# Performance work log

Hardware: AMD Instinct MI355X
Metric: run time of the kernel (lower is better)

## Reference

```python
import jax, jax.numpy as jnp
import numpy as np

NP = 100000   # total patch-graph nodes
NG = 2000     # number of patch graphs == mesh nodes
EP = 800000   # patch edges
NM = 2000     # mesh nodes
EM = 32000    # mesh edges
FIN = 5       # patch_feat_dim
EPS = 1e-5


def _leaky(x, s):
    return jnp.where(x >= 0, x, s * x)


def _gat(x, W, al, ar, src, dst, n):
    # DGL GATConv (no bias/residual, eval mode): per-head projection,
    # additive attention with LeakyReLU(0.2), segment softmax over incoming
    # edges per destination, weighted scatter-sum.
    H, D = al.shape
    h = (x @ W).reshape(n, H, D)                  # [N,H,D]
    el = (h * al).sum(-1)                         # [N,H]
    er = (h * ar).sum(-1)                         # [N,H]
    e = _leaky(el[src] + er[dst], 0.2)            # [E,H]
    m = jax.ops.segment_max(e, dst, num_segments=n)
    ee = jnp.exp(e - m[dst])
    s = jax.ops.segment_sum(ee, dst, num_segments=n)
    a = ee / jnp.maximum(s, 1e-9)[dst]            # [E,H]
    return jax.ops.segment_sum(h[src] * a[:, :, None], dst, num_segments=n)


def _gnorm(x, g, b, al):
    # GraphNorm over all nodes in the batch (called without graph in source)
    mu = x.mean(0, keepdims=True)
    xc = x - al * mu
    v = (xc * xc).mean(0, keepdims=True)
    return g * xc / jnp.sqrt(v + EPS) + b


def setup_inputs() -> dict:
    key = jax.random.key(0)
    ks = jax.random.split(key, 40)
    w = lambda k, sh: jax.random.normal(k, sh, jnp.float32) * 0.1
    d = {}
    d['node_feats'] = jax.random.normal(ks[0], (NP, FIN), jnp.float32)
    d['patch_src'] = jax.random.randint(ks[1], (EP,), 0, NP)
    d['patch_dst'] = jax.random.randint(ks[2], (EP,), 0, NP)
    d['patch_gid'] = jnp.repeat(jnp.arange(NG), NP // NG)  # 50 nodes/graph
    d['mesh_src'] = jax.random.randint(ks[3], (EM,), 0, NM)
    d['mesh_dst'] = jax.random.randint(ks[4], (EM,), 0, NM)
    # PatchReader2GATLayer (hidden=64): GAT1 4h x64, GAT2 3h x64, GATcls 2h x32
    d['pW1'] = w(ks[5], (FIN, 256)); d['pal1'] = w(ks[6], (4, 64)); d['par1'] = w(ks[7], (4, 64))
    d['pg1_g'] = jnp.ones((256,)); d['pg1_b'] = jnp.zeros((256,)); d['pg1_a'] = jnp.ones((256,))
    d['pW2'] = w(ks[8], (256, 192)); d['pal2'] = w(ks[9], (3, 64)); d['par2'] = w(ks[10], (3, 64))
    d['pg2_g'] = jnp.ones((192,)); d['pg2_b'] = jnp.zeros((192,)); d['pg2_a'] = jnp.ones((192,))
    d['pW3'] = w(ks[11], (192, 64)); d['pal3'] = w(ks[12], (2, 32)); d['par3'] = w(ks[13], (2, 32))
    d['pcls'] = w(ks[14], (32, 32))
    # GraphNormPatchReader (readout_dim=32)
    d['rn_g'] = jnp.ones((32,)); d['rn_b'] = jnp.zeros((32,)); d['rn_a'] = jnp.ones((32,))
    # GraphMeshReader2GATLayer (hidden=64): GAT1 4h x64, GAT2 3h x32, GATcls 2h x32
    d['mW1'] = w(ks[15], (32, 256)); d['mal1'] = w(ks[16], (4, 64)); d['mar1'] = w(ks[17], (4, 64))
    d['mg1_g'] = jnp.ones((256,)); d['mg1_b'] = jnp.zeros((256,)); d['mg1_a'] = jnp.ones((256,))
    d['mW2'] = w(ks[18], (256, 96)); d['mal2'] = w(ks[19], (3, 32)); d['mar2'] = w(ks[20], (3, 32))
    d['mg2_g'] = jnp.ones((96,)); d['mg2_b'] = jnp.zeros((96,)); d['mg2_a'] = jnp.ones((96,))
    d['mW3'] = w(ks[21], (96, 64)); d['mal3'] = w(ks[22], (2, 32)); d['mar3'] = w(ks[23], (2, 32))
    d['mcls'] = w(ks[24], (32, 15))
    return d


def reference(node_feats, patch_src, patch_dst, patch_gid, mesh_src, mesh_dst,
              pW1, pal1, par1, pg1_g, pg1_b, pg1_a,
              pW2, pal2, par2, pg2_g, pg2_b, pg2_a,
              pW3, pal3, par3, pcls, rn_g, rn_b, rn_a,
              mW1, mal1, mar1, mg1_g, mg1_b, mg1_a,
              mW2, mal2, mar2, mg2_g, mg2_b, mg2_a,
              mW3, mal3, mar3, mcls):
    # ---- PatchReader2GATLayer over all batched patch graphs ----
    h = _gat(node_feats, pW1, pal1, par1, patch_src, patch_dst, NP).reshape(NP, -1)
    h = _gnorm(_leaky(h, 0.01), pg1_g, pg1_b, pg1_a)
    h = _gat(h, pW2, pal2, par2, patch_src, patch_dst, NP).reshape(NP, -1)
    h = _gnorm(_leaky(h, 0.01), pg2_g, pg2_b, pg2_a)
    h = _gat(h, pW3, pal3, par3, patch_src, patch_dst, NP).mean(1)  # [NP,32]
    cnt = jax.ops.segment_sum(jnp.ones((NP,), h.dtype), patch_gid, num_segments=NG)
    ro = jax.ops.segment_sum(h, patch_gid, num_segments=NG) / jnp.maximum(cnt, 1.0)[:, None]
    ro = ro @ pcls                                 # [NG,32] per-patch readouts
    ro = _gnorm(_leaky(ro, 0.01), rn_g, rn_b, rn_a)
    # ---- GraphMeshReader2GATLayer over mesh graph ----
    m = _gat(ro, mW1, mal1, mar1, mesh_src, mesh_dst, NM).reshape(NM, -1)
    m = _gnorm(_leaky(m, 0.01), mg1_g, mg1_b, mg1_a)
    m = _gat(m, mW2, mal2, mar2, mesh_src, mesh_dst, NM).reshape(NM, -1)
    m = _gnorm(_leaky(m, 0.01), mg2_g, mg2_b, mg2_a)
    m = _gat(m, mW3, mal3, mar3, mesh_src, mesh_dst, NM).mean(1)    # [NM,32]
    mesh_out = m.mean(0, keepdims=True) @ mcls     # dgl.mean_nodes -> [1,15]
    return (mesh_out, ro)
```

## Files before the change

kernel.cpp:

```cpp
#include <hip/hip_runtime.h>

typedef unsigned short ushort;
typedef unsigned int uint;
typedef __attribute__((ext_vector_type(8))) short short8;
typedef __attribute__((ext_vector_type(4))) float float4v;

#define DEV __device__ __forceinline__

DEV float b2f(ushort u) {
    union { uint i; float f; } v; v.i = ((uint)u) << 16; return v.f;
}
DEV ushort f2b(float f) {
    union { float f; uint i; } v; v.f = f;
    uint x = v.i;
    uint r = x + 0x7fffu + ((x >> 16) & 1u);
    return (ushort)(r >> 16);
}
DEV float leaky(float x, float s) { return x >= 0.f ? x : s * x; }

DEV void gload16(const void* g, void* l) {
    __builtin_amdgcn_global_load_lds((const __attribute__((address_space(1))) void*)g,
                                     (__attribute__((address_space(3))) void*)l, 16, 0, 0);
}

struct ConvArgs {
    const void* s[37];
    float* d[37];
    int n[37];
};

__global__ __launch_bounds__(256) void convert_kernel(ConvArgs a, const ushort* __restrict__ x0,
                                                      int* __restrict__ flag) {
    __shared__ int sfp32;
    int tid = threadIdx.x;
    if (tid < 64) {
        int cnt = 0;
        for (int j = 0; j < 8; j++) {
            ushort u = x0[(tid * 8 + j) * 2];
            int e = (u >> 7) & 0xFF;
            if (e >= 100 && e <= 140) cnt++;
        }
#pragma unroll
        for (int m = 1; m < 64; m <<= 1) cnt += __shfl_xor(cnt, m, 64);
        if (tid == 0) sfp32 = (cnt < 256) ? 1 : 0;
    }
    __syncthreads();
    bool fp32 = (sfp32 != 0);
    if (blockIdx.x == 0 && blockIdx.y == 0 && tid == 0) *flag = fp32 ? 1 : 0;

    int ai = blockIdx.y;
    int n = a.n[ai];
    const void* s = a.s[ai];
    float* d = a.d[ai];
    int stride = gridDim.x * blockDim.x;
    if (s == nullptr) {
        for (int i = blockIdx.x * blockDim.x + tid; i < n; i += stride) d[i] = 0.f;
    } else {
        for (int i = blockIdx.x * blockDim.x + tid; i < n; i += stride)
            d[i] = fp32 ? ((const float*)s)[i] : b2f(((const ushort*)s)[i]);
    }
}

struct PackArgs { const float* W; ushort* O; int K; int N; };
struct Pack5 { PackArgs m[5]; };

__global__ __launch_bounds__(256) void pack5_kernel(Pack5 pa) {
    int mi = blockIdx.y;
    const float* __restrict__ W = pa.m[mi].W;
    ushort* __restrict__ O = pa.m[mi].O;
    int K = pa.m[mi].K, N = pa.m[mi].N;
    int G = (K >> 3) * N;
    for (int gi = blockIdx.x * 256 + threadIdx.x; gi < G; gi += gridDim.x * 256) {
        int kb = gi / N;
        int n = gi - kb * N;
        const float* wp = W + (size_t)(kb * 8) * N + n;
        uint4 pk;
        pk.x = (uint)f2b(wp[0]) | ((uint)f2b(wp[N]) << 16);
        pk.y = (uint)f2b(wp[2 * N]) | ((uint)f2b(wp[3 * N]) << 16);
        pk.z = (uint)f2b(wp[4 * N]) | ((uint)f2b(wp[5 * N]) << 16);
        pk.w = (uint)f2b(wp[6 * N]) | ((uint)f2b(wp[7 * N]) << 16);
        *(uint4*)(O + (size_t)gi * 8) = pk;
    }
}

__global__ __launch_bounds__(64) void prep_elr_kernel(const float* __restrict__ W,
                                                      const float* __restrict__ al,
                                                      const float* __restrict__ ar,
                                                      float* __restrict__ wal,
                                                      float* __restrict__ war) {
    int t = threadIdx.x;
    if (t < 20) {
        int k = t >> 2, h = t & 3;
        float sl = 0.f, sr = 0.f;
        for (int d = 0; d < 64; d++) {
            float w = W[k * 256 + h * 64 + d];
            sl += w * al[h * 64 + d];
            sr += w * ar[h * 64 + d];
        }
        wal[t] = sl;
        war[t] = sr;
    }
}

__global__ __launch_bounds__(256) void hist_both(const int* __restrict__ dstP, int* __restrict__ cntP, int EPc,
                                                 const int* __restrict__ dstM, int* __restrict__ cntM, int EMc,
                                                 int PB) {
    bool patch = (int)blockIdx.x < PB;
    const int* dst = patch ? dstP : dstM;
    int* cnt = patch ? cntP : cntM;
    int E = patch ? EPc : EMc;
    int nb = patch ? PB : gridDim.x - PB;
    int b = patch ? blockIdx.x : blockIdx.x - PB;
    int stride = nb * blockDim.x;
    for (int i = b * blockDim.x + threadIdx.x; i < E; i += stride)
        atomicAdd(&cnt[dst[i]], 1);
}

__global__ __launch_bounds__(256) void scan_both(const int* __restrict__ cntP, int* __restrict__ offP,
                                                 int* __restrict__ bsumP, int nP, int SBP,
                                                 const int* __restrict__ cntM, int* __restrict__ offM,
                                                 int* __restrict__ bsumM, int nM) {
    __shared__ int ls[256];
    bool patch = (int)blockIdx.x < SBP;
    const int* cnt = patch ? cntP : cntM;
    int* off = patch ? offP : offM;
    int* bsum = patch ? bsumP : bsumM;
    int n = patch ? nP : nM;
    int b = patch ? blockIdx.x : blockIdx.x - SBP;
    int t = threadIdx.x;
    int base = b * 2048 + t * 8;
    int v[8];
    int s = 0;
#pragma unroll
    for (int i = 0; i < 8; i++) {
        int idx = base + i;
        v[i] = idx < n ? cnt[idx] : 0;
        s += v[i];
    }
    ls[t] = s;
    __syncthreads();
#pragma unroll
    for (int d = 1; d < 256; d <<= 1) {
        int add = (t >= d) ? ls[t - d] : 0;
        __syncthreads();
        ls[t] += add;
        __syncthreads();
    }
    int run = ls[t] - s;
#pragma unroll
    for (int i = 0; i < 8; i++) {
        int idx = base + i;
        if (idx < n) off[idx] = run;
        run += v[i];
// ... 33 lines not shown
                                                    int* __restrict__ csrM, int EMc, int PB) {
    bool patch = (int)blockIdx.x < PB;
    const int* src = patch ? srcP : srcM;
    const int* dst = patch ? dstP : dstM;
    const int* off = patch ? offP : offM;
    int* cursor = patch ? curP : curM;
    int* csr = patch ? csrP : csrM;
    int E = patch ? EPc : EMc;
    int nb = patch ? PB : gridDim.x - PB;
    int b = patch ? blockIdx.x : blockIdx.x - PB;
    int stride = nb * blockDim.x;
    for (int i = b * blockDim.x + threadIdx.x; i < E; i += stride) {
        int d = dst[i];
        int pos = off[d] + atomicAdd(&cursor[d], 1);
        csr[pos] = src[i];
    }
}

__global__ __launch_bounds__(256) void proj1b_kernel(const float* __restrict__ x,
                                                     const float* __restrict__ wal,
                                                     const float* __restrict__ war,
                                                     float* __restrict__ el,
                                                     float* __restrict__ er, int Nn) {
    int n = blockIdx.x * 256 + threadIdx.x;
    if (n >= Nn) return;
    float xv[5];
#pragma unroll
    for (int k = 0; k < 5; k++) xv[k] = x[n * 5 + k];
    float l0 = 0.f, l1 = 0.f, l2 = 0.f, l3 = 0.f;
    float r0 = 0.f, r1 = 0.f, r2 = 0.f, r3 = 0.f;
#pragma unroll
    for (int k = 0; k < 5; k++) {
        float xk = xv[k];
        l0 += xk * wal[k * 4 + 0];
        l1 += xk * wal[k * 4 + 1];
        l2 += xk * wal[k * 4 + 2];
        l3 += xk * wal[k * 4 + 3];
        r0 += xk * war[k * 4 + 0];
        r1 += xk * war[k * 4 + 1];
        r2 += xk * war[k * 4 + 2];
        r3 += xk * war[k * 4 + 3];
    }
    *(float4*)(el + n * 4) = make_float4(l0, l1, l2, l3);
    *(float4*)(er + n * 4) = make_float4(r0, r1, r2, r3);
}

__global__ __launch_bounds__(256, 4) void aggr1_fly_kernel(const float* __restrict__ x,
                                                           const float* __restrict__ W,
                                                           const float* __restrict__ el,
                                                           const float* __restrict__ er,
                                                           const int* __restrict__ off,
                                                           const int* __restrict__ csr,
                                                           float* __restrict__ out,
                                                           float* __restrict__ cstat, int Nn) {
    __shared__ float s1m[4][256];
    __shared__ float s1q[4][256];
    int wid = threadIdx.x >> 6;
    int lane = threadIdx.x & 63;
    int grp = lane / 20;
    int gl = lane - grp * 20;
    int dbase = blockIdx.x * 12 + wid * 3;
    int d = dbase + grp;
    bool accl = (grp < 3) && (d < Nn);
    int dd = accl ? d : 0;
    int h_ = gl / 5, k_ = gl - h_ * 5;
    int c0 = lane * 4;
    int myhead = lane >> 4;
    float w0[5], w1[5], w2[5], w3[5];
#pragma unroll
    for (int k = 0; k < 5; k++) {
        float4 wv = *(const float4*)(W + k * 256 + c0);
        w0[k] = wv.x; w1[k] = wv.y; w2[k] = wv.z; w3[k] = wv.w;
    }
    float erd = accl ? er[dd * 4 + h_] : 0.f;
    float acc = 0.f, sh = 0.f;
    int e = accl ? off[dd] : 0;
    int e1 = accl ? off[dd + 1] : 0;
#define A1_ACC(XV, EV)                                  \
    {                                                   \
        float e0_ = (EV) + erd;                         \
        e0_ = e0_ >= 0.f ? e0_ : 0.2f * e0_;            \
        float w_ = __expf(fminf(e0_, 80.f));            \
        acc += w_ * (XV);                               \
        sh += w_;                                       \
    }
    for (; e + 4 <= e1; e += 4) {
        int s0 = csr[e], s1 = csr[e + 1], s2 = csr[e + 2], s3 = csr[e + 3];
        float x0 = x[s0 * 5 + k_];
        float x1 = x[s1 * 5 + k_];
        float x2 = x[s2 * 5 + k_];
        float x3 = x[s3 * 5 + k_];
        float v0 = el[s0 * 4 + h_];
        float v1 = el[s1 * 4 + h_];
        float v2 = el[s2 * 4 + h_];
        float v3 = el[s3 * 4 + h_];
        A1_ACC(x0, v0) A1_ACC(x1, v1) A1_ACC(x2, v2) A1_ACC(x3, v3)
    }
    for (; e < e1; e++) {
        int s0 = csr[e];
        float x0 = x[s0 * 5 + k_];
        float v0 = el[s0 * 4 + h_];
        A1_ACC(x0, v0)
    }
#undef A1_ACC
    float ls0 = 0.f, ls1 = 0.f, ls2 = 0.f, ls3 = 0.f;
    float lq0 = 0.f, lq1 = 0.f, lq2 = 0.f, lq3 = 0.f;
#pragma unroll
    for (int g3 = 0; g3 < 3; g3++) {
        int dsto = dbase + g3;
        if (dsto >= Nn) break;
        float a_k[5];
#pragma unroll
        for (int k = 0; k < 5; k++) a_k[k] = __shfl(acc, g3 * 20 + myhead * 5 + k, 64);
        float s = __shfl(sh, g3 * 20 + myhead * 5, 64);
        float inv = 1.f / fmaxf(s, 1e-9f);
        float o0 = 0.f, o1 = 0.f, o2 = 0.f, o3 = 0.f;
#pragma unroll
        for (int k = 0; k < 5; k++) {
            o0 += a_k[k] * w0[k]; o1 += a_k[k] * w1[k];
            o2 += a_k[k] * w2[k]; o3 += a_k[k] * w3[k];
        }
        float4 o;
        o.x = leaky(o0 * inv, 0.01f);
        o.y = leaky(o1 * inv, 0.01f);
        o.z = leaky(o2 * inv, 0.01f);
        o.w = leaky(o3 * inv, 0.01f);
        *(float4*)(out + (size_t)dsto * 256 + c0) = o;
        ls0 += o.x; lq0 += o.x * o.x;
        ls1 += o.y; lq1 += o.y * o.y;
        ls2 += o.z; lq2 += o.z * o.z;
        ls3 += o.w; lq3 += o.w * o.w;
    }
    *(float4*)&s1m[wid][c0] = make_float4(ls0, ls1, ls2, ls3);
    *(float4*)&s1q[wid][c0] = make_float4(lq0, lq1, lq2, lq3);
    __syncthreads();
    int tid = threadIdx.x;
    float ssv = 0.f, sqv = 0.f;
#pragma unroll
    for (int w8 = 0; w8 < 4; w8++) { ssv += s1m[w8][tid]; sqv += s1q[w8][tid]; }
    float* dst = cstat + (size_t)(blockIdx.x & 7) * 1024;
    atomicAdd(dst + tid, ssv);
    atomicAdd(dst + 512 + tid, sqv);
}

template <int H, int LOGD, int HD>
__global__ __launch_bounds__(256, 4) void aggr4_kernel(const ushort* __restrict__ h,
                                                       const float* __restrict__ el,
                                                       const float* __restrict__ er,
                                                       const int* __restrict__ off,
                                                       const int* __restrict__ csr,
                                                       float* __restrict__ out,
                                                       float* __restrict__ cstat, int Nn,
                                                       float oslope) {
    __shared__ float ssm[8][HD];
    __shared__ float ssq[8][HD];
    int wid = threadIdx.x >> 6;
    int lane = threadIdx.x & 63;
    int half = lane >> 5, hl = lane & 31;
    constexpr int NL = HD / 8;
    int d = blockIdx.x * 8 + wid * 2 + half;
    bool valid = (hl < NL) && (d < Nn);
    int dd = valid ? d : 0;
    int myhead = (hl * 8) >> LOGD;
    float erd = valid ? er[dd * H + myhead] : 0.f;
    float a0 = 0.f, a1 = 0.f, a2 = 0.f, a3 = 0.f;
    float a4 = 0.f, a5 = 0.f, a6 = 0.f, a7 = 0.f, s = 0.f;
    int e = valid ? off[dd] : 0;
    int e1 = valid ? off[dd + 1] : 0;
#define A8_ACC(EV, HR)                                      \
    {                                                       \
        float ev_ = (EV) + erd;                             \
        ev_ = ev_ >= 0.f ? ev_ : 0.2f * ev_;                \
        float w_ = __expf(fminf(ev_, 80.f));                \
        a0 += w_ * b2f((ushort)(HR).x);                     \
        a1 += w_ * b2f((ushort)((HR).x >> 16));             \
        a2 += w_ * b2f((ushort)(HR).y);                     \
        a3 += w_ * b2f((ushort)((HR).y >> 16));             \
        a4 += w_ * b2f((ushort)(HR).z);                     \
        a5 += w_ * b2f((ushort)((HR).z >> 16));             \
        a6 += w_ * b2f((ushort)(HR).w);                     \
        a7 += w_ * b2f((ushort)((HR).w >> 16));             \
        s += w_;                                            \
    }
#define A8_ACCM(OK, EV, HR)                                 \
    {                                                       \
        float ev_ = (EV) + erd;                             \
        ev_ = ev_ >= 0.f ? ev_ : 0.2f * ev_;                \
        float w_ = (OK) ? __expf(fminf(ev_, 80.f)) : 0.f;   \
        a0 += w_ * b2f((ushort)(HR).x);                     \
        a1 += w_ * b2f((ushort)((HR).x >> 16));             \
        a2 += w_ * b2f((ushort)(HR).y);                     \
        a3 += w_ * b2f((ushort)((HR).y >> 16));             \
        a4 += w_ * b2f((ushort)(HR).z);                     \
        a5 += w_ * b2f((ushort)((HR).z >> 16));             \
        a6 += w_ * b2f((ushort)(HR).w);                     \
        a7 += w_ * b2f((ushort)((HR).w >> 16));             \
        s += w_;                                            \
    }
    for (; e + 4 <= e1; e += 4) {
        int s0 = csr[e], s1 = csr[e + 1], s2 = csr[e + 2], s3 = csr[e + 3];
        float e0 = el[s0 * H + myhead];
        float e1v = el[s1 * H + myhead];
        float e2v = el[s2 * H + myhead];
        float e3v = el[s3 * H + myhead];
        uint4 h0 = *(const uint4*)(h + (size_t)s0 * HD + hl * 8);
        uint4 h1 = *(const uint4*)(h + (size_t)s1 * HD + hl * 8);
        uint4 h2 = *(const uint4*)(h + (size_t)s2 * HD + hl * 8);
        uint4 h3 = *(const uint4*)(h + (size_t)s3 * HD + hl * 8);
        A8_ACC(e0, h0) A8_ACC(e1v, h1) A8_ACC(e2v, h2) A8_ACC(e3v, h3)
    }
    if (e < e1) {
        bool k1 = e + 1 < e1, k2 = e + 2 < e1, k3 = e + 3 < e1;
        int s0 = csr[e];
        int s1 = csr[k1 ? e + 1 : e];
        int s2 = csr[k2 ? e + 2 : e];
        int s3 = csr[k3 ? e + 3 : e];
        float e0 = el[s0 * H + myhead];
        float e1v = el[s1 * H + myhead];
        float e2v = el[s2 * H + myhead];
        float e3v = el[s3 * H + myhead];
        uint4 h0 = *(const uint4*)(h + (size_t)s0 * HD + hl * 8);
        uint4 h1 = *(const uint4*)(h + (size_t)s1 * HD + hl * 8);
        uint4 h2 = *(const uint4*)(h + (size_t)s2 * HD + hl * 8);
        uint4 h3 = *(const uint4*)(h + (size_t)s3 * HD + hl * 8);
        A8_ACCM(true, e0, h0) A8_ACCM(k1, e1v, h1) A8_ACCM(k2, e2v, h2) A8_ACCM(k3, e3v, h3)
    }
#undef A8_ACC
#undef A8_ACCM
    float o0 = 0.f, o1 = 0.f, o2 = 0.f, o3 = 0.f;
    float o4 = 0.f, o5 = 0.f, o6 = 0.f, o7 = 0.f;
    if (valid) {
        float inv = 1.f / fmaxf(s, 1e-9f);
        o0 = leaky(a0 * inv, oslope);
        o1 = leaky(a1 * inv, oslope);
        o2 = leaky(a2 * inv, oslope);
        o3 = leaky(a3 * inv, oslope);
        o4 = leaky(a4 * inv, oslope);
        o5 = leaky(a5 * inv, oslope);
        o6 = leaky(a6 * inv, oslope);
        o7 = leaky(a7 * inv, oslope);
        float* po = out + (size_t)dd * HD + hl * 8;
        *(float4*)(po) = make_float4(o0, o1, o2, o3);
        *(float4*)(po + 4) = make_float4(o4, o5, o6, o7);
    }
    int r = wid * 2 + half;
    if (hl < NL) {
        int cb = hl * 8;
        *(float4*)&ssm[r][cb] = make_float4(o0, o1, o2, o3);
        *(float4*)&ssm[r][cb + 4] = make_float4(o4, o5, o6, o7);
        *(float4*)&ssq[r][cb] = make_float4(o0 * o0, o1 * o1, o2 * o2, o3 * o3);
        *(float4*)&ssq[r][cb + 4] = make_float4(o4 * o4, o5 * o5, o6 * o6, o7 * o7);
    }
    __syncthreads();
    int tid = threadIdx.x;
    if (tid < HD) {
        float sv = 0.f, qv = 0.f;
#pragma unroll
        for (int rr = 0; rr < 8; rr++) { sv += ssm[rr][tid]; qv += ssq[rr][tid]; }
        float* dst = cstat + (size_t)(blockIdx.x & 7) * 1024;
        atomicAdd(dst + tid, sv);
        atomicAdd(dst + 512 + tid, qv);
    }
}

__global__ __launch_bounds__(256, 4) void aggr_mean_kernel(const ushort* __restrict__ h,
                                                           const float* __restrict__ el,
                                                           const float* __restrict__ er,
                                                           const int* __restrict__ off,
                                                           const int* __restrict__ csr,
                                                           const int* __restrict__ gid,
                                                           float* __restrict__ out_sum,
                                                           float* __restrict__ out_cnt,
                                                           int Nn) {
    __shared__ float red[8][32];
    __shared__ int gids[8];
    int wid = threadIdx.x >> 6;
    int lane = threadIdx.x & 63;
    int half = lane >> 5;
    int hl = lane & 31;
    int row = wid * 2 + half;
    int d = blockIdx.x * 8 + row;
    bool valid = d < Nn;
    int dd = valid ? d : 0;
    int head = hl >> 4;
    float erd = er[dd * 2 + head];
    float a0 = 0.f, a1 = 0.f, s = 0.f;
    int e = valid ? off[dd] : 0;
    int e1 = valid ? off[dd + 1] : 0;
#define AM_ACC(Q, V)                                        \
    {                                                       \
        float ev_ = (head ? (Q).y : (Q).x) + erd;           \
        ev_ = ev_ >= 0.f ? ev_ : 0.2f * ev_;                \
        float w_ = __expf(fminf(ev_, 80.f));                \
        a0 += w_ * b2f((ushort)(V));                        \
        a1 += w_ * b2f((ushort)((V) >> 16));                \
        s += w_;                                            \
    }
#define AM_ACCM(OK, Q, V)                                   \
    {                                                       \
        float ev_ = (head ? (Q).y : (Q).x) + erd;           \
        ev_ = ev_ >= 0.f ? ev_ : 0.2f * ev_;                \
        float w_ = (OK) ? __expf(fminf(ev_, 80.f)) : 0.f;   \
        a0 += w_ * b2f((ushort)(V));                        \
        a1 += w_ * b2f((ushort)((V) >> 16));                \
// ... 45 lines not shown
        uint v2 = *(const uint*)(h + (size_t)s2 * 64 + hl * 2);
        uint v3 = *(const uint*)(h + (size_t)s3 * 64 + hl * 2);
        uint v4 = *(const uint*)(h + (size_t)s4 * 64 + hl * 2);
        uint v5 = *(const uint*)(h + (size_t)s5 * 64 + hl * 2);
        uint v6 = *(const uint*)(h + (size_t)s6 * 64 + hl * 2);
        uint v7 = *(const uint*)(h + (size_t)s7 * 64 + hl * 2);
        AM_ACCM(true, q0, v0) AM_ACCM(k1, q1, v1) AM_ACCM(k2, q2, v2) AM_ACCM(k3, q3, v3)
        AM_ACCM(k4, q4, v4) AM_ACCM(k5, q5, v5) AM_ACCM(k6, q6, v6) AM_ACCM(k7, q7, v7)
    }
#undef AM_ACC
#undef AM_ACCM
    float inv = 1.f / fmaxf(s, 1e-9f);
    float y0 = a0 * inv, y1 = a1 * inv;
    float p0 = __shfl(y0, lane + 16, 64);
    float p1 = __shfl(y1, lane + 16, 64);
    if (hl < 16) {
        red[row][2 * hl] = valid ? 0.5f * (y0 + p0) : 0.f;
        red[row][2 * hl + 1] = valid ? 0.5f * (y1 + p1) : 0.f;
        if (hl == 0) gids[row] = valid ? (gid ? gid[d] : 0) : -1;
    }
    __syncthreads();
    if (threadIdx.x < 32) {
        int c = threadIdx.x;
        float sum = 0.f;
        int cur = gids[0];
#pragma unroll
        for (int r = 0; r < 8; r++) {
            int gr = gids[r];
            if (gr != cur) {
                if (cur >= 0) atomicAdd(&out_sum[cur * 32 + c], sum);
                sum = 0.f;
                cur = gr;
            }
            if (gr >= 0) sum += red[r][c];
        }
        if (cur >= 0) atomicAdd(&out_sum[cur * 32 + c], sum);
    } else if (threadIdx.x == 32 && out_cnt) {
        float cnt = 0.f;
        int cur = gids[0];
#pragma unroll
        for (int r = 0; r < 8; r++) {
            int gr = gids[r];
            if (gr != cur) {
                if (cur >= 0) atomicAdd(&out_cnt[cur], cnt);
                cnt = 0.f;
                cur = gr;
            }
            if (gr >= 0) cnt += 1.f;
        }
        if (cur >= 0) atomicAdd(&out_cnt[cur], cnt);
    }
}

__global__ void gnorm_apply_ro_kernel(const float* __restrict__ x,
                                      const float* __restrict__ cstat,
                                      const float* __restrict__ g,
                                      const float* __restrict__ b,
                                      const float* __restrict__ a,
                                      void* __restrict__ doutv,
                                      const int* __restrict__ flag,
                                      float* __restrict__ rof, int Nn) {
    int c = threadIdx.x;
    float cs = 0.f, cq = 0.f;
#pragma unroll
    for (int s8 = 0; s8 < 8; s8++) {
        cs += cstat[s8 * 1024 + c];
        cq += cstat[s8 * 1024 + 512 + c];
    }
    float invn = 1.f / (float)Nn;
    float mu = cs * invn, ex2 = cq * invn;
    float av = a[c];
    float var = ex2 - 2.f * av * mu * mu + av * av * mu * mu;
    float sc = g[c] * rsqrtf(var + 1e-5f);
    float sh = b[c] - sc * av * mu;
    bool fp32 = (*flag != 0);
    for (int r = blockIdx.x; r < Nn; r += gridDim.x) {
        int i = r * 32 + c;
        float v = x[i] * sc + sh;
        rof[i] = v;
        if (fp32) ((float*)doutv)[15 + i] = v;
        else      ((ushort*)doutv)[15 + i] = f2b(v);
    }
}

__global__ __launch_bounds__(256) void readout_kernel(const float* __restrict__ ro_sum,
                                                      const float* __restrict__ ro_cnt,
                                                      const float* __restrict__ pcls,
                                                      float* __restrict__ ro_lin,
                                                      float* __restrict__ cstat, int NGc) {
    __shared__ float ss[32], sq[32];
    int tid = threadIdx.x;
    if (tid < 32) { ss[tid] = 0.f; sq[tid] = 0.f; }
    __syncthreads();
    int idx = blockIdx.x * 256 + tid;
    int g = idx >> 5, c = idx & 31;
    float v = 0.f;
    if (g < NGc) {
        float inv = 1.f / fmaxf(ro_cnt[g], 1.f);
        float acc = 0.f;
#pragma unroll
        for (int k = 0; k < 32; k++) acc += ro_sum[g * 32 + k] * inv * pcls[k * 32 + c];
        v = leaky(acc, 0.01f);
        ro_lin[g * 32 + c] = v;
    }
    atomicAdd(&ss[c], v);
    atomicAdd(&sq[c], v * v);
    __syncthreads();
    if (tid < 32) {
        float* dst = cstat + (size_t)(blockIdx.x & 7) * 1024;
        atomicAdd(dst + tid, ss[tid]);
        atomicAdd(dst + 512 + tid, sq[tid]);
    }
}

template <int K, int N, int H, int LOGD, bool GN>
__global__ __launch_bounds__(256, 4) void gemm_bf_kernel(const float* __restrict__ A,
                                                         const ushort* __restrict__ Bc,
                                                         const float* __restrict__ csum,
                                                         const float* __restrict__ g,
                                                         const float* __restrict__ gb,
                                                         const float* __restrict__ ga,
                                                         const float* __restrict__ al,
                                                         const float* __restrict__ ar,
                                                         ushort* __restrict__ C,
                                                         float* __restrict__ el,
                                                         float* __restrict__ er, int M) {
    constexpr int NT = N / 16;
    constexpr int T = K / 32;
    constexpr int BG = 4 * N;
    constexpr int RB = (BG + 255) / 256;
    __shared__ __align__(16) ushort Blds[2][BG * 8];
    __shared__ float ScL[K], ShL[K];
    int tid = threadIdx.x;
    int w = tid >> 6, lane = tid & 63, q = lane >> 4, l16 = lane & 15;
    int m0 = blockIdx.x * 64;
    if constexpr (GN) {
        if (tid < K) {
            float cs = 0.f, cq = 0.f;
#pragma unroll
            for (int s8 = 0; s8 < 8; s8++) {
                cs += csum[s8 * 1024 + tid];
                cq += csum[s8 * 1024 + 512 + tid];
            }
            float invn = 1.f / (float)M;
            float mu = cs * invn, ex2 = cq * invn;
            float av = ga[tid];
            float var = ex2 - 2.f * av * mu * mu + av * av * mu * mu;
            float sc = g[tid] * rsqrtf(var + 1e-5f);
            ScL[tid] = sc;
            ShL[tid] = gb[tid] - sc * av * mu;
        }
    }
    int row = m0 + w * 16 + l16;
    const float* ap = A + (size_t)(row < M ? row : 0) * K + q * 8;

#pragma unroll
    for (int rb = 0; rb < RB; rb++) {
        int gidx = rb * 256 + tid;
        if (BG % 256 == 0 || gidx < BG) gload16(Bc + (size_t)gidx * 8, &Blds[0][gidx * 8]);
    }
    float4 a0 = *(const float4*)(ap);
    float4 a1 = *(const float4*)(ap + 4);
    float4v acc[NT];
#pragma unroll
// ... 140 lines not shown
    float* elm = (float*)alloc((size_t)NM * 4 * 4);
    float* erm = (float*)alloc((size_t)NM * 4 * 4);
    float* ro_lin = (float*)alloc((size_t)NG * 32 * 4);
    float* ro_f = (float*)alloc((size_t)NG * 32 * 4);
    ushort* Bp2 = (ushort*)alloc(256 * 192 * 2);
    ushort* Bp3 = (ushort*)alloc(192 * 64 * 2);
    ushort* Bm1 = (ushort*)alloc(32 * 256 * 2);
    ushort* Bm2 = (ushort*)alloc(256 * 96 * 2);
    ushort* Bm3 = (ushort*)alloc(96 * 64 * 2);
    float* wal1 = (float*)alloc(20 * 4);
    float* war1 = (float*)alloc(20 * 4);

    ConvArgs ca;
    float* convp[36];
    int conv_idx[36];
    conv_idx[0] = 0;
    for (int i = 1; i < 36; i++) conv_idx[i] = 5 + i;
    for (int j = 0; j < 36; j++) {
        int ii = conv_idx[j];
        int n = in_sizes[ii];
        float* dd = (float*)alloc((size_t)n * 4);
        ca.s[j] = d_in[ii];
        ca.d[j] = dd;
        ca.n[j] = n;
        convp[j] = dd;
    }
    ca.s[36] = nullptr;
    ca.d[36] = (float*)zbase;
    ca.n[36] = (int)(zbytes / 4);

    const float* xf = convp[0];
    const float *pW1f = convp[1], *pal1f = convp[2], *par1f = convp[3];
    const float *pg1_gf = convp[4], *pg1_bf = convp[5], *pg1_af = convp[6];
    const float *pW2f = convp[7], *pal2f = convp[8], *par2f = convp[9];
    const float *pg2_gf = convp[10], *pg2_bf = convp[11], *pg2_af = convp[12];
    const float *pW3f = convp[13], *pal3f = convp[14], *par3f = convp[15];
    const float* pclsf = convp[16];
    const float *rn_gf = convp[17], *rn_bf2 = convp[18], *rn_af = convp[19];
    const float *mW1f = convp[20], *mal1f = convp[21], *mar1f = convp[22];
    const float *mg1_gf = convp[23], *mg1_bf = convp[24], *mg1_af = convp[25];
    const float *mW2f = convp[26], *mal2f = convp[27], *mar2f = convp[28];
    const float *mg2_gf = convp[29], *mg2_bf = convp[30], *mg2_af = convp[31];
    const float *mW3f = convp[32], *mal3f = convp[33], *mar3f = convp[34];
    const float* mclsf = convp[35];

    convert_kernel<<<dim3(16, 37), 256, 0, stream>>>(ca, (const ushort*)d_in[0], flag);

    Pack5 p5;
    p5.m[0] = {pW2f, Bp2, 256, 192};
    p5.m[1] = {pW3f, Bp3, 192, 64};
    p5.m[2] = {mW1f, Bm1, 32, 256};
    p5.m[3] = {mW2f, Bm2, 256, 96};
    p5.m[4] = {mW3f, Bm3, 96, 64};
    pack5_kernel<<<dim3(48, 5), 256, 0, stream>>>(p5);
    prep_elr_kernel<<<1, 64, 0, stream>>>(pW1f, pal1f, par1f, wal1, war1);

    const int SBP = (NP + 2047) / 2048, SBM = (NM + 2047) / 2048;
    hist_both<<<512 + 64, 256, 0, stream>>>(patch_dst, cnt_p, EP, mesh_dst, cnt_m, EM, 512);
    scan_both<<<SBP + SBM, 256, 0, stream>>>(cnt_p, off_p, bsum_p, NP, SBP, cnt_m, off_m, bsum_m, NM);
    fixup_both<<<SBP + SBM, 256, 0, stream>>>(bsum_p, off_p, NP, SBP, bsum_m, off_m, NM, SBM);
    scatter_both<<<512 + 64, 256, 0, stream>>>(patch_src, patch_dst, off_p, cursor_p, csr_p, EP,
                                               mesh_src, mesh_dst, off_m, cursor_m, csr_m, EM, 512);

    int gP12 = (NP + 11) / 12;
    int gA2 = (NP + 7) / 8, gA2m = (NM + 7) / 8;
    int gP2 = (NP + 7) / 8, gM2 = (NM + 7) / 8;
    int gT = (NP + 63) / 64, gTm = (NM + 63) / 64;
    float* cb0 = colbuf + 0 * 8192;
    float* cb1 = colbuf + 1 * 8192;
    float* cb2 = colbuf + 2 * 8192;
    float* cb3 = colbuf + 3 * 8192;
    float* cb4 = colbuf + 4 * 8192;

    proj1b_kernel<<<(NP + 255) / 256, 256, 0, stream>>>(xf, wal1, war1, el, er, NP);
    aggr1_fly_kernel<<<gP12, 256, 0, stream>>>(xf, pW1f, el, er, off_p, csr_p, gbuf, cb0, NP);

    gemm_bf_kernel<256, 192, 3, 6, true><<<gT, 256, 0, stream>>>(
        gbuf, Bp2, cb0, pg1_gf, pg1_bf, pg1_af, pal2f, par2f, hbuf, el, er, NP);
    aggr4_kernel<3, 6, 192><<<gA2, 256, 0, stream>>>(hbuf, el, er, off_p, csr_p, gbuf, cb1, NP, 0.01f);

    gemm_bf_kernel<192, 64, 2, 5, true><<<gT, 256, 0, stream>>>(
        gbuf, Bp3, cb1, pg2_gf, pg2_bf, pg2_af, pal3f, par3f, hbuf, el, er, NP);
    aggr_mean_kernel<<<gP2, 256, 0, stream>>>(hbuf, el, er, off_p, csr_p, patch_gid,
                                              ro_sum, ro_cnt, NP);

    readout_kernel<<<(NG * 32 + 255) / 256, 256, 0, stream>>>(ro_sum, ro_cnt, pclsf, ro_lin, cb2, NG);
    gnorm_apply_ro_kernel<<<64, 32, 0, stream>>>(ro_lin, cb2, rn_gf, rn_bf2, rn_af,
                                                 d_out, flag, ro_f, NG);

    gemm_bf_kernel<32, 256, 4, 6, false><<<gTm, 256, 0, stream>>>(
        ro_f, Bm1, nullptr, nullptr, nullptr, nullptr, mal1f, mar1f, hm, elm, erm, NM);
    aggr4_kernel<4, 6, 256><<<gA2m, 256, 0, stream>>>(hm, elm, erm, off_m, csr_m, gm, cb3, NM, 0.01f);

    gemm_bf_kernel<256, 96, 3, 5, true><<<gTm, 256, 0, stream>>>(
        gm, Bm2, cb3, mg1_gf, mg1_bf, mg1_af, mal2f, mar2f, hm, elm, erm, NM);
    aggr4_kernel<3, 5, 96><<<gA2m, 256, 0, stream>>>(hm, elm, erm, off_m, csr_m, gm, cb4, NM, 0.01f);

    gemm_bf_kernel<96, 64, 2, 5, true><<<gTm, 256, 0, stream>>>(
        gm, Bm3, cb4, mg2_gf, mg2_bf, mg2_af, mal3f, mar3f, hm, elm, erm, NM);
    aggr_mean_kernel<<<gM2, 256, 0, stream>>>(hm, elm, erm, off_m, csr_m, nullptr,
                                              msum, nullptr, NM);
    final_kernel<<<1, 64, 0, stream>>>(msum, mclsf, d_out, flag, NM);

    (void)n_in; (void)out_size; (void)ws_size;
}
```

Baseline: 559.5 us.

## Grid-stride aggregation kernels and merge small prep/readout launches

```diff
diff --git a/kernel.cpp b/kernel.cpp
--- a/kernel.cpp
+++ b/kernel.cpp
@@ -62,10 +62,29 @@
 }
 
 struct PackArgs { const float* W; ushort* O; int K; int N; };
-struct Pack5 { PackArgs m[5]; };
+struct Pack5 {
+    PackArgs m[5];
+    const float *W1, *al1, *ar1;
+    float *wal, *war;
+};
 
 __global__ __launch_bounds__(256) void pack5_kernel(Pack5 pa) {
     int mi = blockIdx.y;
+    if (mi == 5) {
+        if (blockIdx.x == 0 && threadIdx.x < 20) {
+            int t = threadIdx.x;
+            int k = t >> 2, h = t & 3;
+            float sl = 0.f, sr = 0.f;
+            for (int d = 0; d < 64; d++) {
+                float w = pa.W1[k * 256 + h * 64 + d];
+                sl += w * pa.al1[h * 64 + d];
+                sr += w * pa.ar1[h * 64 + d];
+            }
+            pa.wal[t] = sl;
+            pa.war[t] = sr;
+        }
+        return;
+    }
     const float* __restrict__ W = pa.m[mi].W;
     ushort* __restrict__ O = pa.m[mi].O;
     int K = pa.m[mi].K, N = pa.m[mi].N;
@@ -80,25 +99,6 @@
         pk.z = (uint)f2b(wp[4 * N]) | ((uint)f2b(wp[5 * N]) << 16);
         pk.w = (uint)f2b(wp[6 * N]) | ((uint)f2b(wp[7 * N]) << 16);
         *(uint4*)(O + (size_t)gi * 8) = pk;
-    }
-}
-
-__global__ __launch_bounds__(64) void prep_elr_kernel(const float* __restrict__ W,
-                                                      const float* __restrict__ al,
-                                                      const float* __restrict__ ar,
-                                                      float* __restrict__ wal,
-                                                      float* __restrict__ war) {
-    int t = threadIdx.x;
-    if (t < 20) {
-        int k = t >> 2, h = t & 3;
-        float sl = 0.f, sr = 0.f;
-        for (int d = 0; d < 64; d++) {
-            float w = W[k * 256 + h * 64 + d];
-            sl += w * al[h * 64 + d];
-            sr += w * ar[h * 64 + d];
-        }
-        wal[t] = sl;
-        war[t] = sr;
     }
 }
 
@@ -238,17 +238,14 @@
                                                            const int* __restrict__ off,
                                                            const int* __restrict__ csr,
                                                            float* __restrict__ out,
-                                                           float* __restrict__ cstat, int Nn) {
+                                                           float* __restrict__ cstat,
+                                                           int ntiles, int Nn) {
     __shared__ float s1m[4][256];
     __shared__ float s1q[4][256];
     int wid = threadIdx.x >> 6;
     int lane = threadIdx.x & 63;
     int grp = lane / 20;
     int gl = lane - grp * 20;
-    int dbase = blockIdx.x * 12 + wid * 3;
-    int d = dbase + grp;
-    bool accl = (grp < 3) && (d < Nn);
-    int dd = accl ? d : 0;
     int h_ = gl / 5, k_ = gl - h_ * 5;
     int c0 = lane * 4;
     int myhead = lane >> 4;
@@ -258,10 +255,18 @@
         float4 wv = *(const float4*)(W + k * 256 + c0);
         w0[k] = wv.x; w1[k] = wv.y; w2[k] = wv.z; w3[k] = wv.w;
     }
-    float erd = accl ? er[dd * 4 + h_] : 0.f;
-    float acc = 0.f, sh = 0.f;
-    int e = accl ? off[dd] : 0;
-    int e1 = accl ? off[dd + 1] : 0;
+    float ls0 = 0.f, ls1 = 0.f, ls2 = 0.f, ls3 = 0.f;
+    float lq0 = 0.f, lq1 = 0.f, lq2 = 0.f, lq3 = 0.f;
+
+    for (int tile = blockIdx.x; tile < ntiles; tile += gridDim.x) {
+        int dbase = tile * 12 + wid * 3;
+        int d = dbase + grp;
+        bool accl = (grp < 3) && (d < Nn);
+        int dd = accl ? d : 0;
+        float erd = accl ? er[dd * 4 + h_] : 0.f;
+        float acc = 0.f, sh = 0.f;
+        int e = accl ? off[dd] : 0;
+        int e1 = accl ? off[dd + 1] : 0;
 #define A1_ACC(XV, EV)                                  \
     {                                                   \
         float e0_ = (EV) + erd;                         \
@@ -270,52 +275,51 @@
         acc += w_ * (XV);                               \
         sh += w_;                                       \
     }
-    for (; e + 4 <= e1; e += 4) {
-        int s0 = csr[e], s1 = csr[e + 1], s2 = csr[e + 2], s3 = csr[e + 3];
-        float x0 = x[s0 * 5 + k_];
-        float x1 = x[s1 * 5 + k_];
-        float x2 = x[s2 * 5 + k_];
-        float x3 = x[s3 * 5 + k_];
-        float v0 = el[s0 * 4 + h_];
-        float v1 = el[s1 * 4 + h_];
-        float v2 = el[s2 * 4 + h_];
-        float v3 = el[s3 * 4 + h_];
-        A1_ACC(x0, v0) A1_ACC(x1, v1) A1_ACC(x2, v2) A1_ACC(x3, v3)
-    }
-    for (; e < e1; e++) {
-        int s0 = csr[e];
-        float x0 = x[s0 * 5 + k_];
-        float v0 = el[s0 * 4 + h_];
-        A1_ACC(x0, v0)
-    }
+        for (; e + 4 <= e1; e += 4) {
+            int s0 = csr[e], s1 = csr[e + 1], s2 = csr[e + 2], s3 = csr[e + 3];
+            float x0 = x[s0 * 5 + k_];
+            float x1 = x[s1 * 5 + k_];
+            float x2 = x[s2 * 5 + k_];
+            float x3 = x[s3 * 5 + k_];
+            float v0 = el[s0 * 4 + h_];
+            float v1 = el[s1 * 4 + h_];
+            float v2 = el[s2 * 4 + h_];
+            float v3 = el[s3 * 4 + h_];
+            A1_ACC(x0, v0) A1_ACC(x1, v1) A1_ACC(x2, v2) A1_ACC(x3, v3)
+        }
+        for (; e < e1; e++) {
+            int s0 = csr[e];
+            float x0 = x[s0 * 5 + k_];
+            float v0 = el[s0 * 4 + h_];
+            A1_ACC(x0, v0)
+        }
 #undef A1_ACC
-    float ls0 = 0.f, ls1 = 0.f, ls2 = 0.f, ls3 = 0.f;
-    float lq0 = 0.f, lq1 = 0.f, lq2 = 0.f, lq3 = 0.f;
-#pragma unroll
-    for (int g3 = 0; g3 < 3; g3++) {
-        int dsto = dbase + g3;
-        if (dsto >= Nn) break;
-        float a_k[5];
-#pragma unroll
-        for (int k = 0; k < 5; k++) a_k[k] = __shfl(acc, g3 * 20 + myhead * 5 + k, 64);
-        float s = __shfl(sh, g3 * 20 + myhead * 5, 64);
-        float inv = 1.f / fmaxf(s, 1e-9f);
-        float o0 = 0.f, o1 = 0.f, o2 = 0.f, o3 = 0.f;
-#pragma unroll
-        for (int k = 0; k < 5; k++) {
-            o0 += a_k[k] * w0[k]; o1 += a_k[k] * w1[k];
-            o2 += a_k[k] * w2[k]; o3 += a_k[k] * w3[k];
-        }
-        float4 o;
-        o.x = leaky(o0 * inv, 0.01f);
-        o.y = leaky(o1 * inv, 0.01f);
-        o.z = leaky(o2 * inv, 0.01f);
-        o.w = leaky(o3 * inv, 0.01f);
-        *(float4*)(out + (size_t)dsto * 256 + c0) = o;
-        ls0 += o.x; lq0 += o.x * o.x;
-        ls1 += o.y; lq1 += o.y * o.y;
-        ls2 += o.z; lq2 += o.z * o.z;
-        ls3 += o.w; lq3 += o.w * o.w;
+#pragma unroll
+        for (int g3 = 0; g3 < 3; g3++) {
+            int dsto = dbase + g3;
+            if (dsto >= Nn) break;
+            float a_k[5];
+#pragma unroll
+            for (int k = 0; k < 5; k++) a_k[k] = __shfl(acc, g3 * 20 + myhead * 5 + k, 64);
+            float s = __shfl(sh, g3 * 20 + myhead * 5, 64);
+            float inv = 1.f / fmaxf(s, 1e-9f);
+            float o0 = 0.f, o1 = 0.f, o2 = 0.f, o3 = 0.f;
+#pragma unroll
+            for (int k = 0; k < 5; k++) {
+                o0 += a_k[k] * w0[k]; o1 += a_k[k] * w1[k];
+                o2 += a_k[k] * w2[k]; o3 += a_k[k] * w3[k];
+            }
+            float4 o;
+            o.x = leaky(o0 * inv, 0.01f);
+            o.y = leaky(o1 * inv, 0.01f);
+            o.z = leaky(o2 * inv, 0.01f);
+            o.w = leaky(o3 * inv, 0.01f);
+            *(float4*)(out + (size_t)dsto * 256 + c0) = o;
+            ls0 += o.x; lq0 += o.x * o.x;
+            ls1 += o.y; lq1 += o.y * o.y;
+            ls2 += o.z; lq2 += o.z * o.z;
+            ls3 += o.w; lq3 += o.w * o.w;
+        }
     }
     *(float4*)&s1m[wid][c0] = make_float4(ls0, ls1, ls2, ls3);
     *(float4*)&s1q[wid][c0] = make_float4(lq0, lq1, lq2, lq3);
@@ -336,7 +340,8 @@
                                                        const int* __restrict__ off,
                                                        const int* __restrict__ csr,
                                                        float* __restrict__ out,
-                                                       float* __restrict__ cstat, int Nn,
+                                                       float* __restrict__ cstat,
+                                                       int ntiles, int Nn,
                                                        float oslope) {
     __shared__ float ssm[8][HD];
     __shared__ float ssq[8][HD];
@@ -344,15 +349,21 @@
     int lane = threadIdx.x & 63;
     int half = lane >> 5, hl = lane & 31;
     constexpr int NL = HD / 8;
-    int d = blockIdx.x * 8 + wid * 2 + half;
-    bool valid = (hl < NL) && (d < Nn);
-    int dd = valid ? d : 0;
     int myhead = (hl * 8) >> LOGD;
-    float erd = valid ? er[dd * H + myhead] : 0.f;
-    float a0 = 0.f, a1 = 0.f, a2 = 0.f, a3 = 0.f;
-    float a4 = 0.f, a5 = 0.f, a6 = 0.f, a7 = 0.f, s = 0.f;
-    int e = valid ? off[dd] : 0;
-    int e1 = valid ? off[dd + 1] : 0;
+    float rs0 = 0.f, rs1 = 0.f, rs2 = 0.f, rs3 = 0.f;
+    float rs4 = 0.f, rs5 = 0.f, rs6 = 0.f, rs7 = 0.f;
+    float rq0 = 0.f, rq1 = 0.f, rq2 = 0.f, rq3 = 0.f;
+    float rq4 = 0.f, rq5 = 0.f, rq6 = 0.f, rq7 = 0.f;
+
+    for (int tile = blockIdx.x; tile < ntiles; tile += gridDim.x) {
+        int d = tile * 8 + wid * 2 + half;
+        bool valid = (hl < NL) && (d < Nn);
+        int dd = valid ? d : 0;
+        float erd = valid ? er[dd * H + myhead] : 0.f;
+        float a0 = 0.f, a1 = 0.f, a2 = 0.f, a3 = 0.f;
+        float a4 = 0.f, a5 = 0.f, a6 = 0.f, a7 = 0.f, s = 0.f;
+        int e = valid ? off[dd] : 0;
+        int e1 = valid ? off[dd + 1] : 0;
 #define A8_ACC(EV, HR)                                      \
     {                                                       \
         float ev_ = (EV) + erd;                             \
@@ -383,59 +394,66 @@
         a7 += w_ * b2f((ushort)((HR).w >> 16));             \
         s += w_;                                            \
     }
-    for (; e + 4 <= e1; e += 4) {
-        int s0 = csr[e], s1 = csr[e + 1], s2 = csr[e + 2], s3 = csr[e + 3];
-        float e0 = el[s0 * H + myhead];
-        float e1v = el[s1 * H + myhead];
-        float e2v = el[s2 * H + myhead];
-        float e3v = el[s3 * H + myhead];
-        uint4 h0 = *(const uint4*)(h + (size_t)s0 * HD + hl * 8);
-        uint4 h1 = *(const uint4*)(h + (size_t)s1 * HD + hl * 8);
-        uint4 h2 = *(const uint4*)(h + (size_t)s2 * HD + hl * 8);
-        uint4 h3 = *(const uint4*)(h + (size_t)s3 * HD + hl * 8);
-        A8_ACC(e0, h0) A8_ACC(e1v, h1) A8_ACC(e2v, h2) A8_ACC(e3v, h3)
-    }
-    if (e < e1) {
-        bool k1 = e + 1 < e1, k2 = e + 2 < e1, k3 = e + 3 < e1;
-        int s0 = csr[e];
-        int s1 = csr[k1 ? e + 1 : e];
-        int s2 = csr[k2 ? e + 2 : e];
-        int s3 = csr[k3 ? e + 3 : e];
-        float e0 = el[s0 * H + myhead];
-        float e1v = el[s1 * H + myhead];
-        float e2v = el[s2 * H + myhead];
-        float e3v = el[s3 * H + myhead];
-        uint4 h0 = *(const uint4*)(h + (size_t)s0 * HD + hl * 8);
-        uint4 h1 = *(const uint4*)(h + (size_t)s1 * HD + hl * 8);
-        uint4 h2 = *(const uint4*)(h + (size_t)s2 * HD + hl * 8);
-        uint4 h3 = *(const uint4*)(h + (size_t)s3 * HD + hl * 8);
-        A8_ACCM(true, e0, h0) A8_ACCM(k1, e1v, h1) A8_ACCM(k2, e2v, h2) A8_ACCM(k3, e3v, h3)
-    }
+        for (; e + 4 <= e1; e += 4) {
+            int s0 = csr[e], s1 = csr[e + 1], s2 = csr[e + 2], s3 = csr[e + 3];
+            float e0 = el[s0 * H + myhead];
+            float e1v = el[s1 * H + myhead];
+            float e2v = el[s2 * H + myhead];
+            float e3v = el[s3 * H + myhead];
+            uint4 h0 = *(const uint4*)(h + (size_t)s0 * HD + hl * 8);
+            uint4 h1 = *(const uint4*)(h + (size_t)s1 * HD + hl * 8);
+            uint4 h2 = *(const uint4*)(h + (size_t)s2 * HD + hl * 8);
+            uint4 h3 = *(const uint4*)(h + (size_t)s3 * HD + hl * 8);
+            A8_ACC(e0, h0) A8_ACC(e1v, h1) A8_ACC(e2v, h2) A8_ACC(e3v, h3)
+        }
+        if (e < e1) {
+            bool k1 = e + 1 < e1, k2 = e + 2 < e1, k3 = e + 3 < e1;
+            int s0 = csr[e];
+            int s1 = csr[k1 ? e + 1 : e];
+            int s2 = csr[k2 ? e + 2 : e];
+            int s3 = csr[k3 ? e + 3 : e];
+            float e0 = el[s0 * H + myhead];
+            float e1v = el[s1 * H + myhead];
+            float e2v = el[s2 * H + myhead];
+            float e3v = el[s3 * H + myhead];
+            uint4 h0 = *(const uint4*)(h + (size_t)s0 * HD + hl * 8);
+            uint4 h1 = *(const uint4*)(h + (size_t)s1 * HD + hl * 8);
+            uint4 h2 = *(const uint4*)(h + (size_t)s2 * HD + hl * 8);
+            uint4 h3 = *(const uint4*)(h + (size_t)s3 * HD + hl * 8);
+            A8_ACCM(true, e0, h0) A8_ACCM(k1, e1v, h1) A8_ACCM(k2, e2v, h2) A8_ACCM(k3, e3v, h3)
+        }
 #undef A8_ACC
 #undef A8_ACCM
-    float o0 = 0.f, o1 = 0.f, o2 = 0.f, o3 = 0.f;
-    float o4 = 0.f, o5 = 0.f, o6 = 0.f, o7 = 0.f;
-    if (valid) {
-        float inv = 1.f / fmaxf(s, 1e-9f);
-        o0 = leaky(a0 * inv, oslope);
-        o1 = leaky(a1 * inv, oslope);
-        o2 = leaky(a2 * inv, oslope);
-        o3 = leaky(a3 * inv, oslope);
-        o4 = leaky(a4 * inv, oslope);
-        o5 = leaky(a5 * inv, oslope);
-        o6 = leaky(a6 * inv, oslope);
-        o7 = leaky(a7 * inv, oslope);
-        float* po = out + (size_t)dd * HD + hl * 8;
-        *(float4*)(po) = make_float4(o0, o1, o2, o3);
-        *(float4*)(po + 4) = make_float4(o4, o5, o6, o7);
+        if (valid) {
+            float inv = 1.f / fmaxf(s, 1e-9f);
+            float o0 = leaky(a0 * inv, oslope);
+            float o1 = leaky(a1 * inv, oslope);
+            float o2 = leaky(a2 * inv, oslope);
+            float o3 = leaky(a3 * inv, oslope);
+            float o4 = leaky(a4 * inv, oslope);
+            float o5 = leaky(a5 * inv, oslope);
+            float o6 = leaky(a6 * inv, oslope);
+            float o7 = leaky(a7 * inv, oslope);
+            float* po = out + (size_t)dd * HD + hl * 8;
+            *(float4*)(po) = make_float4(o0, o1, o2, o3);
+            *(float4*)(po + 4) = make_float4(o4, o5, o6, o7);
+            rs0 += o0; rq0 += o0 * o0;
+            rs1 += o1; rq1 += o1 * o1;
+            rs2 += o2; rq2 += o2 * o2;
+            rs3 += o3; rq3 += o3 * o3;
+            rs4 += o4; rq4 += o4 * o4;
+            rs5 += o5; rq5 += o5 * o5;
+            rs6 += o6; rq6 += o6 * o6;
+            rs7 += o7; rq7 += o7 * o7;
+        }
     }
     int r = wid * 2 + half;
     if (hl < NL) {
         int cb = hl * 8;
-        *(float4*)&ssm[r][cb] = make_float4(o0, o1, o2, o3);
-        *(float4*)&ssm[r][cb + 4] = make_float4(o4, o5, o6, o7);
-        *(float4*)&ssq[r][cb] = make_float4(o0 * o0, o1 * o1, o2 * o2, o3 * o3);
-        *(float4*)&ssq[r][cb + 4] = make_float4(o4 * o4, o5 * o5, o6 * o6, o7 * o7);
+        *(float4*)&ssm[r][cb] = make_float4(rs0, rs1, rs2, rs3);
+        *(float4*)&ssm[r][cb + 4] = make_float4(rs4, rs5, rs6, rs7);
+        *(float4*)&ssq[r][cb] = make_float4(rq0, rq1, rq2, rq3);
+        *(float4*)&ssq[r][cb + 4] = make_float4(rq4, rq5, rq6, rq7);
     }
     __syncthreads();
     int tid = threadIdx.x;
@@ -587,64 +605,58 @@
     }
 }
 
-__global__ void gnorm_apply_ro_kernel(const float* __restrict__ x,
-                                      const float* __restrict__ cstat,
-                                      const float* __restrict__ g,
-                                      const float* __restrict__ b,
-                                      const float* __restrict__ a,
-                                      void* __restrict__ doutv,
-                                      const int* __restrict__ flag,
-                                      float* __restrict__ rof, int Nn) {
-    int c = threadIdx.x;
-    float cs = 0.f, cq = 0.f;
-#pragma unroll
-    for (int s8 = 0; s8 < 8; s8++) {
-        cs += cstat[s8 * 1024 + c];
-        cq += cstat[s8 * 1024 + 512 + c];
-    }
-    float invn = 1.f / (float)Nn;
-    float mu = cs * invn, ex2 = cq * invn;
-    float av = a[c];
-    float var = ex2 - 2.f * av * mu * mu + av * av * mu * mu;
-    float sc = g[c] * rsqrtf(var + 1e-5f);
-    float sh = b[c] - sc * av * mu;
-    bool fp32 = (*flag != 0);
-    for (int r = blockIdx.x; r < Nn; r += gridDim.x) {
-        int i = r * 32 + c;
-        float v = x[i] * sc + sh;
-        rof[i] = v;
-        if (fp32) ((float*)doutv)[15 + i] = v;
-        else      ((ushort*)doutv)[15 + i] = f2b(v);
-    }
-}
-
-__global__ __launch_bounds__(256) void readout_kernel(const float* __restrict__ ro_sum,
-                                                      const float* __restrict__ ro_cnt,
-                                                      const float* __restrict__ pcls,
-                                                      float* __restrict__ ro_lin,
-                                                      float* __restrict__ cstat, int NGc) {
-    __shared__ float ss[32], sq[32];
+__global__ __launch_bounds__(1024) void readout_gnorm_kernel(const float* __restrict__ ro_sum,
+                                                             const float* __restrict__ ro_cnt,
+                                                             const float* __restrict__ pcls,
+                                                             const float* __restrict__ g,
+                                                             const float* __restrict__ b,
+                                                             const float* __restrict__ a,
+                                                             void* __restrict__ doutv,
+                                                             const int* __restrict__ flag,
+                                                             float* __restrict__ ro_lin,
+                                                             float* __restrict__ rof, int NGc) {
+    __shared__ float pc[1024];
+    __shared__ float ssum[32][33];
+    __shared__ float ssq2[32][33];
+    __shared__ float scl[32], shl[32];
     int tid = threadIdx.x;
-    if (tid < 32) { ss[tid] = 0.f; sq[tid] = 0.f; }
+    pc[tid] = pcls[tid];
+    int rgrp = tid >> 5, c = tid & 31;
+    float ls = 0.f, lq = 0.f;
     __syncthreads();
-    int idx = blockIdx.x * 256 + tid;
-    int g = idx >> 5, c = idx & 31;
-    float v = 0.f;
-    if (g < NGc) {
-        float inv = 1.f / fmaxf(ro_cnt[g], 1.f);
+    for (int idx = tid; idx < NGc * 32; idx += 1024) {
+        int gg = idx >> 5;
+        float inv = 1.f / fmaxf(ro_cnt[gg], 1.f);
         float acc = 0.f;
 #pragma unroll
-        for (int k = 0; k < 32; k++) acc += ro_sum[g * 32 + k] * inv * pcls[k * 32 + c];
-        v = leaky(acc, 0.01f);
-        ro_lin[g * 32 + c] = v;
-    }
-    atomicAdd(&ss[c], v);
-    atomicAdd(&sq[c], v * v);
+        for (int k = 0; k < 32; k++) acc += ro_sum[gg * 32 + k] * inv * pc[k * 32 + c];
+        float v = leaky(acc, 0.01f);
+        ro_lin[idx] = v;
+        ls += v; lq += v * v;
+    }
+    ssum[rgrp][c] = ls;
+    ssq2[rgrp][c] = lq;
     __syncthreads();
     if (tid < 32) {
-        float* dst = cstat + (size_t)(blockIdx.x & 7) * 1024;
-        atomicAdd(dst + tid, ss[tid]);
-        atomicAdd(dst + 512 + tid, sq[tid]);
+        float cs = 0.f, cq = 0.f;
+#pragma unroll
+        for (int r = 0; r < 32; r++) { cs += ssum[r][tid]; cq += ssq2[r][tid]; }
+        float invn = 1.f / (float)NGc;
+        float mu = cs * invn, ex2 = cq * invn;
+        float av = a[tid];
+        float var = ex2 - 2.f * av * mu * mu + av * av * mu * mu;
+        float sc = g[tid] * rsqrtf(var + 1e-5f);
+        scl[tid] = sc;
+        shl[tid] = b[tid] - sc * av * mu;
+    }
+    __syncthreads();
+    bool fp32 = (*flag != 0);
+    float sc = scl[c], sh = shl[c];
+    for (int idx = tid; idx < NGc * 32; idx += 1024) {
+        float v = ro_lin[idx] * sc + sh;
+        rof[idx] = v;
+        if (fp32) ((float*)doutv)[15 + idx] = v;
+        else      ((ushort*)doutv)[15 + idx] = f2b(v);
     }
 }
 
@@ -891,8 +903,9 @@
     p5.m[2] = {mW1f, Bm1, 32, 256};
     p5.m[3] = {mW2f, Bm2, 256, 96};
     p5.m[4] = {mW3f, Bm3, 96, 64};
-    pack5_kernel<<<dim3(48, 5), 256, 0, stream>>>(p5);
-    prep_elr_kernel<<<1, 64, 0, stream>>>(pW1f, pal1f, par1f, wal1, war1);
+    p5.W1 = pW1f; p5.al1 = pal1f; p5.ar1 = par1f;
+    p5.wal = wal1; p5.war = war1;
+    pack5_kernel<<<dim3(48, 6), 256, 0, stream>>>(p5);
 
     const int SBP = (NP + 2047) / 2048, SBM = (NM + 2047) / 2048;
     hist_both<<<512 + 64, 256, 0, stream>>>(patch_dst, cnt_p, EP, mesh_dst, cnt_m, EM, 512);
@@ -901,39 +914,40 @@
     scatter_both<<<512 + 64, 256, 0, stream>>>(patch_src, patch_dst, off_p, cursor_p, csr_p, EP,
                                                mesh_src, mesh_dst, off_m, cursor_m, csr_m, EM, 512);
 
-    int gP12 = (NP + 11) / 12;
-    int gA2 = (NP + 7) / 8, gA2m = (NM + 7) / 8;
+    int t1 = (NP + 11) / 12;
+    int g1 = t1 < 2048 ? t1 : 2048;
+    int tA = (NP + 7) / 8;
+    int gA = tA < 2048 ? tA : 2048;
+    int tAm = (NM + 7) / 8;
     int gP2 = (NP + 7) / 8, gM2 = (NM + 7) / 8;
     int gT = (NP + 63) / 64, gTm = (NM + 63) / 64;
     float* cb0 = colbuf + 0 * 8192;
     float* cb1 = colbuf + 1 * 8192;
-    float* cb2 = colbuf + 2 * 8192;
     float* cb3 = colbuf + 3 * 8192;
     float* cb4 = colbuf + 4 * 8192;
 
     proj1b_kernel<<<(NP + 255) / 256, 256, 0, stream>>>(xf, wal1, war1, el, er, NP);
-    aggr1_fly_kernel<<<gP12, 256, 0, stream>>>(xf, pW1f, el, er, off_p, csr_p, gbuf, cb0, NP);
+    aggr1_fly_kernel<<<g1, 256, 0, stream>>>(xf, pW1f, el, er, off_p, csr_p, gbuf, cb0, t1, NP);
 
     gemm_bf_kernel<256, 192, 3, 6, true><<<gT, 256, 0, stream>>>(
         gbuf, Bp2, cb0, pg1_gf, pg1_bf, pg1_af, pal2f, par2f, hbuf, el, er, NP);
-    aggr4_kernel<3, 6, 192><<<gA2, 256, 0, stream>>>(hbuf, el, er, off_p, csr_p, gbuf, cb1, NP, 0.01f);
+    aggr4_kernel<3, 6, 192><<<gA, 256, 0, stream>>>(hbuf, el, er, off_p, csr_p, gbuf, cb1, tA, NP, 0.01f);
 
     gemm_bf_kernel<192, 64, 2, 5, true><<<gT, 256, 0, stream>>>(
         gbuf, Bp3, cb1, pg2_gf, pg2_bf, pg2_af, pal3f, par3f, hbuf, el, er, NP);
     aggr_mean_kernel<<<gP2, 256, 0, stream>>>(hbuf, el, er, off_p, csr_p, patch_gid,
                                               ro_sum, ro_cnt, NP);
 
-    readout_kernel<<<(NG * 32 + 255) / 256, 256, 0, stream>>>(ro_sum, ro_cnt, pclsf, ro_lin, cb2, NG);
-    gnorm_apply_ro_kernel<<<64, 32, 0, stream>>>(ro_lin, cb2, rn_gf, rn_bf2, rn_af,
-                                                 d_out, flag, ro_f, NG);
+    readout_gnorm_kernel<<<1, 1024, 0, stream>>>(ro_sum, ro_cnt, pclsf, rn_gf, rn_bf2, rn_af,
+                                                 d_out, flag, ro_lin, ro_f, NG);
 
     gemm_bf_kernel<32, 256, 4, 6, false><<<gTm, 256, 0, stream>>>(
         ro_f, Bm1, nullptr, nullptr, nullptr, nullptr, mal1f, mar1f, hm, elm, erm, NM);
-    aggr4_kernel<4, 6, 256><<<gA2m, 256, 0, stream>>>(hm, elm, erm, off_m, csr_m, gm, cb3, NM, 0.01f);
+    aggr4_kernel<4, 6, 256><<<tAm, 256, 0, stream>>>(hm, elm, erm, off_m, csr_m, gm, cb3, tAm, NM, 0.01f);
 
     gemm_bf_kernel<256, 96, 3, 5, true><<<gTm, 256, 0, stream>>>(
         gm, Bm2, cb3, mg1_gf, mg1_bf, mg1_af, mal2f, mar2f, hm, elm, erm, NM);
-    aggr4_kernel<3, 5, 96><<<gA2m, 256, 0, stream>>>(hm, elm, erm, off_m, csr_m, gm, cb4, NM, 0.01f);
+    aggr4_kernel<3, 5, 96><<<tAm, 256, 0, stream>>>(hm, elm, erm, off_m, csr_m, gm, cb4, tAm, NM, 0.01f);
 
     gemm_bf_kernel<96, 64, 2, 5, true><<<gTm, 256, 0, stream>>>(
         gm, Bm3, cb4, mg2_gf, mg2_bf, mg2_af, mal3f, mar3f, hm, elm, erm, NM);
```

Result: slower. 663.3 us (+18.5%).
